# Performance work log

Hardware: AMD Instinct MI355X
Metric: run time of the kernel (lower is better)

The kernel has to match this reference:

```python
import jax, jax.numpy as jnp
import numpy as np

BATCH, N_AGENTS, OBS_DIM, ACTOR_DIM, N_ACTIONS = 8192, 64, 128, 64, 32


def setup_inputs() -> dict:
    key = jax.random.key(0)
    ks = jax.random.split(key, 14)
    s = 0.05
    inp = {
        "O": jax.random.normal(ks[0], (BATCH, N_AGENTS, OBS_DIM), dtype=jnp.float32),
        "W_enc": jax.random.normal(ks[1], (OBS_DIM, ACTOR_DIM), dtype=jnp.float32) * s,
        "b_enc": jax.random.normal(ks[2], (ACTOR_DIM,), dtype=jnp.float32) * s,
        "W1": jax.random.normal(ks[3], (2 * ACTOR_DIM, ACTOR_DIM), dtype=jnp.float32) * s,
        "b1": jax.random.normal(ks[4], (ACTOR_DIM,), dtype=jnp.float32) * s,
        "W2": jax.random.normal(ks[5], (2 * ACTOR_DIM, ACTOR_DIM), dtype=jnp.float32) * s,
        "b2": jax.random.normal(ks[6], (ACTOR_DIM,), dtype=jnp.float32) * s,
        "W3": jax.random.normal(ks[7], (2 * ACTOR_DIM, ACTOR_DIM), dtype=jnp.float32) * s,
        "b3": jax.random.normal(ks[8], (ACTOR_DIM,), dtype=jnp.float32) * s,
        "W4": jax.random.normal(ks[9], (2 * ACTOR_DIM, ACTOR_DIM), dtype=jnp.float32) * s,
        "b4": jax.random.normal(ks[10], (ACTOR_DIM,), dtype=jnp.float32) * s,
        "W_dec": jax.random.normal(ks[11], (N_AGENTS * ACTOR_DIM, N_ACTIONS), dtype=jnp.float32) * s,
        "b_dec": jax.random.normal(ks[12], (N_ACTIONS,), dtype=jnp.float32) * s,
    }
    return inp


def _comm_layer(H, W, b, n_agents):
    # get_commvar: masked mean over other agents, but divided by n_agents
    # (the zeroed self term is included in the mean denominator) ->
    # C_i = (sum_j H_j - H_i) / n_agents, exactly equal to the original math.
    C = (jnp.sum(H, axis=1, keepdims=True) - H) / n_agents  # [B, A, D]
    Hcat = jnp.concatenate([H, C], axis=-1)                 # [B, A, 2D]
    return Hcat @ W + b                                     # no activation (faithful)


def reference(O, W_enc, b_enc, W1, b1, W2, b2, W3, b3, W4, b4, W_dec, b_dec):
    B, A, _ = O.shape
    H = jax.nn.sigmoid(O @ W_enc + b_enc)  # [B, A, D]
    H = _comm_layer(H, W1, b1, A)
    H = _comm_layer(H, W2, b2, A)
    H = _comm_layer(H, W3, b3, A)
    H = _comm_layer(H, W4, b4, A)
    Hf = H.reshape(B, -1)                  # [B, A*D]
    return Hf @ W_dec + b_dec              # [B, n_actions]
```

## Files before the change

kernel.cpp:

```cpp
#include <hip/hip_runtime.h>
#include <hip/hip_bf16.h>
#include <stdint.h>


#define BATCHN 8192

typedef __attribute__((ext_vector_type(8))) short short8;
typedef __attribute__((ext_vector_type(4))) float floatx4;

__device__ __forceinline__ unsigned short f2b(float f) {
    union { float f; uint32_t u; } v; v.f = f;
    uint32_t r = v.u + 0x7FFFu + ((v.u >> 16) & 1u);
    return (unsigned short)(r >> 16);
}

__device__ __forceinline__ uint32_t pk2(float x, float y) {
    float2 t; t.x = x; t.y = y;
    __hip_bfloat162 h = __float22bfloat162_rn(t);
    union { __hip_bfloat162 h; uint32_t u; } c; c.h = h;
    return c.u;
}

#define U16_WENC 0
#define U16_WCAT 8192
#define U16_WSUM 40960
#define U16_WDEC 57344
#define U16_H4   188416

__global__ __launch_bounds__(256) void prep_kernel(
    const float* __restrict__ Wenc,
    const float* __restrict__ W1, const float* __restrict__ W2,
    const float* __restrict__ W3, const float* __restrict__ W4,
    const float* __restrict__ Wdec,
    unsigned short* __restrict__ ws)
{
    int tid = blockIdx.x * 256 + threadIdx.x;
    const float* WL[4] = {W1, W2, W3, W4};
    if (tid < 8192) {
        int n = tid >> 7, k = tid & 127;
        ws[U16_WENC + n*128 + k] = f2b(Wenc[k*64 + n]);
    } else if (tid < 40960) {
        int e = tid - 8192;
        int l = e >> 13, r = e & 8191;
        int n = r >> 7, k = r & 127;
        const float* W = WL[l];
        float v = W[k*64 + n];
        if (k < 64) v -= W[(k+64)*64 + n] * (1.0f/64.0f);
        ws[U16_WCAT + l*8192 + n*128 + k] = f2b(v);
    } else if (tid < 57344) {
        int e = tid - 40960;
        int l = e >> 12, r = e & 4095;
        int f = r >> 6, k = r & 63;
        const float* W = WL[l];
        float v = W[k*64 + f] + W[(k+64)*64 + f] * (63.0f/64.0f);
        ws[U16_WSUM + l*4096 + f*64 + k] = f2b(v);
    } else {
        int e = tid - 57344;
        int n = e >> 12, k = e & 4095;
        ws[U16_WDEC + n*4096 + k] = f2b(Wdec[k*32 + n]);
    }
}

__global__ __launch_bounds__(256, 3) void fused3_kernel(
    const float* __restrict__ O,
    const unsigned short* __restrict__ WencT,
    const unsigned short* __restrict__ WcatT,
    const unsigned short* __restrict__ WsumT,
    const float* __restrict__ b_enc,
    const float* __restrict__ b1, const float* __restrict__ b2,
    const float* __restrict__ b3, const float* __restrict__ b4,
    unsigned short* __restrict__ H4out)
{
    __shared__ unsigned short sG[4][64*72];
    __shared__ unsigned short sS[4][64];

    const int t = threadIdx.x, lane = t & 63, w = t >> 6;
    const int m = lane & 15, q = lane >> 4;
    const int b = blockIdx.x * 4 + w;
    unsigned short* myG = sG[w];
    unsigned short* myS = sS[w];

    floatx4 acc[4][4];
    floatx4 bb[4];

    #pragma unroll
    for (int ft = 0; ft < 4; ft++) {
        float4 bv = *(const float4*)(b_enc + ft*16 + q*4);
        bb[ft] = (floatx4){bv.x, bv.y, bv.z, bv.w};
    }
    #pragma unroll
    for (int ft = 0; ft < 4; ft++)
        #pragma unroll
        for (int at = 0; at < 4; at++)
            acc[ft][at] = bb[ft];

    const float* Ob = O + (size_t)b * 8192;
    #pragma unroll
    for (int s = 0; s < 4; s++) {
        short8 Wf[4], Bf[4];
        #pragma unroll
        for (int ft = 0; ft < 4; ft++)
            Wf[ft] = *(const short8*)(WencT + (ft*16+m)*128 + s*32 + q*8);
        #pragma unroll
        for (int at = 0; at < 4; at++) {
            const float* pr = Ob + (at*16+m)*128 + s*32 + q*8;
            float4 f0 = *(const float4*)pr;
            float4 f1 = *(const float4*)(pr + 4);
            uint32_t* pa = (uint32_t*)&Bf[at];
            pa[0] = pk2(f0.x, f0.y); pa[1] = pk2(f0.z, f0.w);
            pa[2] = pk2(f1.x, f1.y); pa[3] = pk2(f1.z, f1.w);
        }
        #pragma unroll
        for (int ft = 0; ft < 4; ft++)
            #pragma unroll
            for (int at = 0; at < 4; at++)
                acc[ft][at] = __builtin_amdgcn_mfma_f32_16x16x32_bf16(Wf[ft], Bf[at], acc[ft][at], 0, 0, 0);
    }
    #pragma unroll
    for (int ft = 0; ft < 4; ft++)
        #pragma unroll
        for (int at = 0; at < 4; at++)
            #pragma unroll
            for (int r = 0; r < 4; r++)
                acc[ft][at][r] = 1.0f / (1.0f + __expf(-acc[ft][at][r]));

    #pragma unroll
    for (int ft = 0; ft < 4; ft++) {
        float tr[4];
        #pragma unroll
        for (int r = 0; r < 4; r++)
            tr[r] = acc[ft][0][r] + acc[ft][1][r] + acc[ft][2][r] + acc[ft][3][r];
        #pragma unroll
        for (int msk = 1; msk <= 8; msk <<= 1)
            #pragma unroll
            for (int r = 0; r < 4; r++)
                tr[r] += __shfl_xor(tr[r], msk, 64);
        uint2 d;
        d.x = pk2(tr[0] * (1.0f/64.0f), tr[1] * (1.0f/64.0f));
        d.y = pk2(tr[2] * (1.0f/64.0f), tr[3] * (1.0f/64.0f));
        if (m == 0) *(uint2*)&myS[ft*16 + q*4] = d;
    }
    #pragma unroll
    for (int ft = 0; ft < 4; ft++)
        #pragma unroll
        for (int at = 0; at < 4; at++) {
            uint2 d;
            d.x = pk2(acc[ft][at][0], acc[ft][at][1]);
            d.y = pk2(acc[ft][at][2], acc[ft][at][3]);
            *(uint2*)&myG[(at*16+m)*72 + ft*16 + q*4] = d;
        }

    const float* bs_[4] = {b1, b2, b3, b4};
    #pragma unroll
    for (int l = 0; l < 4; l++) {
        const unsigned short* Wl  = WcatT + l*8192;
        const unsigned short* Wsl = WsumT + l*4096;
        const float* bp = bs_[l];
        #pragma unroll
        for (int ft = 0; ft < 4; ft++) {
            float4 bv = *(const float4*)(bp + ft*16 + q*4);
            bb[ft] = (floatx4){bv.x, bv.y, bv.z, bv.w};
        }
        short8 Sf[2];
        #pragma unroll
        for (int s2 = 0; s2 < 2; s2++)
            Sf[s2] = *(const short8*)&myS[s2*32 + q*8];

        #pragma unroll
        for (int ft = 0; ft < 4; ft++)
            #pragma unroll
            for (int at = 0; at < 4; at++)
                acc[ft][at] = bb[ft];

        #pragma unroll
        for (int s2 = 0; s2 < 2; s2++) {
            short8 Wf[4], Gf[4];
            #pragma unroll
            for (int ft = 0; ft < 4; ft++)
                Wf[ft] = *(const short8*)(Wl + (ft*16+m)*128 + s2*32 + q*8);
            #pragma unroll
            for (int at = 0; at < 4; at++)
                Gf[at] = *(const short8*)&myG[(at*16+m)*72 + s2*32 + q*8];
            #pragma unroll
            for (int ft = 0; ft < 4; ft++)
                #pragma unroll
                for (int at = 0; at < 4; at++)
                    acc[ft][at] = __builtin_amdgcn_mfma_f32_16x16x32_bf16(Wf[ft], Gf[at], acc[ft][at], 0, 0, 0);
        }
        #pragma unroll
        for (int s2 = 0; s2 < 2; s2++) {
            short8 Wf[4];
            #pragma unroll
            for (int ft = 0; ft < 4; ft++)
                Wf[ft] = *(const short8*)(Wl + (ft*16+m)*128 + (2+s2)*32 + q*8);
            #pragma unroll
            for (int ft = 0; ft < 4; ft++)
                #pragma unroll
                for (int at = 0; at < 4; at++)
                    acc[ft][at] = __builtin_amdgcn_mfma_f32_16x16x32_bf16(Wf[ft], Sf[s2], acc[ft][at], 0, 0, 0);
        }

        if (l < 3) {
            floatx4 sacc[4];
            #pragma unroll
            for (int ft = 0; ft < 4; ft++) sacc[ft] = (floatx4){0.f, 0.f, 0.f, 0.f};
            #pragma unroll
            for (int s2 = 0; s2 < 2; s2++) {
                #pragma unroll
                for (int ft = 0; ft < 4; ft++) {
                    short8 Wsf = *(const short8*)(Wsl + (ft*16+m)*64 + s2*32 + q*8);
                    sacc[ft] = __builtin_amdgcn_mfma_f32_16x16x32_bf16(Wsf, Sf[s2], sacc[ft], 0, 0, 0);
                }
            }
            #pragma unroll
            for (int ft = 0; ft < 4; ft++) {
                uint2 d;
                d.x = pk2(sacc[ft][0] + bb[ft][0], sacc[ft][1] + bb[ft][1]);
                d.y = pk2(sacc[ft][2] + bb[ft][2], sacc[ft][3] + bb[ft][3]);
                if (m == 0) *(uint2*)&myS[ft*16 + q*4] = d;
            }
            #pragma unroll
            for (int ft = 0; ft < 4; ft++)
                #pragma unroll
                for (int at = 0; at < 4; at++) {
                    uint2 d;
                    d.x = pk2(acc[ft][at][0], acc[ft][at][1]);
                    d.y = pk2(acc[ft][at][2], acc[ft][at][3]);
                    *(uint2*)&myG[(at*16+m)*72 + ft*16 + q*4] = d;
                }
        } else {
            unsigned short* Hb = H4out + (size_t)b * 4096;
            #pragma unroll
            for (int ft = 0; ft < 4; ft++)
                #pragma unroll
                for (int at = 0; at < 4; at++) {
                    uint2 d;
                    d.x = pk2(acc[ft][at][0], acc[ft][at][1]);
                    d.y = pk2(acc[ft][at][2], acc[ft][at][3]);
                    *(uint2*)(Hb + (at*16+m)*64 + ft*16 + q*4) = d;
                }
        }
    }
}

__global__ __launch_bounds__(256) void dec_kernel(
    const unsigned short* __restrict__ Hf,
    const unsigned short* __restrict__ WdecT,
    const float* __restrict__ b_dec,
    float* __restrict__ out)
{
    int gt = blockIdx.x * 256 + threadIdx.x;
    int wave = gt >> 6;
    int lane = gt & 63;
    int rb = wave >> 3;
    int kc = wave & 7;
    int m = lane & 15, q = lane >> 4;

    const unsigned short* aP  = Hf    + (size_t)(rb*16 + m)*4096 + kc*512 + q*8;
    const unsigned short* bP0 = WdecT + (size_t)m*4096        + kc*512 + q*8;
    const unsigned short* bP1 = WdecT + (size_t)(16 + m)*4096 + kc*512 + q*8;

    floatx4 a0 = {0.f, 0.f, 0.f, 0.f}, a1 = {0.f, 0.f, 0.f, 0.f};
    #pragma unroll 4
    for (int s = 0; s < 16; s++) {
        short8 av  = *(const short8*)(aP  + s*32);
        short8 b0v = *(const short8*)(bP0 + s*32);
        short8 b1v = *(const short8*)(bP1 + s*32);
        a0 = __builtin_amdgcn_mfma_f32_16x16x32_bf16(av, b0v, a0, 0, 0, 0);
        a1 = __builtin_amdgcn_mfma_f32_16x16x32_bf16(av, b1v, a1, 0, 0, 0);
    }
    float bias0 = (kc == 0) ? b_dec[m]      : 0.0f;
    float bias1 = (kc == 0) ? b_dec[16 + m] : 0.0f;
    #pragma unroll
    for (int r = 0; r < 4; r++) {
        int row = rb*16 + q*4 + r;
        atomicAdd(&out[row*32 + m],      a0[r] + bias0);
        atomicAdd(&out[row*32 + 16 + m], a1[r] + bias1);
    }
}

extern "C" void kernel_launch(void* const* d_in, const int* in_sizes, int n_in,
                              void* d_out, int out_size, void* d_ws, size_t ws_size,
                              hipStream_t stream)
{
    const float* O    = (const float*)d_in[0];
    const float* Wenc = (const float*)d_in[1];
    const float* benc = (const float*)d_in[2];
    const float* W1   = (const float*)d_in[3];
    const float* b1   = (const float*)d_in[4];
    const float* W2   = (const float*)d_in[5];
    const float* b2   = (const float*)d_in[6];
    const float* W3   = (const float*)d_in[7];
    const float* b3   = (const float*)d_in[8];
    const float* W4   = (const float*)d_in[9];
    const float* b4   = (const float*)d_in[10];
    const float* Wdec = (const float*)d_in[11];
    const float* bdec = (const float*)d_in[12];
    float* out = (float*)d_out;
    unsigned short* ws = (unsigned short*)d_ws;

    hipMemsetAsync(d_out, 0, (size_t)out_size * sizeof(float), stream);
    prep_kernel<<<736, 256, 0, stream>>>(Wenc, W1, W2, W3, W4, Wdec, ws);
    fused3_kernel<<<2048, 256, 0, stream>>>(O, ws + U16_WENC, ws + U16_WCAT,
                                            ws + U16_WSUM,
                                            benc, b1, b2, b3, b4, ws + U16_H4);
    dec_kernel<<<1024, 256, 0, stream>>>(ws + U16_H4, ws + U16_WDEC, bdec, out);
}
```

Before: 502.0 us.

## Prefetch encoder inputs, reorder comm-layer loads, replace decoder atomics with partial-sum reduction

The encoder loop now double-buffers the fp32 observation loads, fetching the next K-slice while the current one is converted and multiplied. Each comm layer loads all G fragments and weights up front and computes the summary vector before the main MFMA block. The decoder splits K into 16 chunks that write partial sums to workspace instead of using atomics, and a new reduction kernel adds the bias and sums the partials. This removes the memset and the atomic contention, at the cost of an extra launch, 16 MB of partial traffic and higher register pressure.

New measurement: 499.9 us. Within noise of the previous version (-0.4%).

```diff
diff --git a/kernel.cpp b/kernel.cpp
--- a/kernel.cpp
+++ b/kernel.cpp
@@ -26,6 +26,7 @@
 #define U16_WSUM 40960
 #define U16_WDEC 57344
 #define U16_H4   188416
+#define F32_PART 16871424
 
 __global__ __launch_bounds__(256) void prep_kernel(
     const float* __restrict__ Wenc,
@@ -61,7 +62,7 @@
     }
 }
 
-__global__ __launch_bounds__(256, 3) void fused3_kernel(
+__global__ __launch_bounds__(256, 3) void fused4_kernel(
     const float* __restrict__ O,
     const unsigned short* __restrict__ WencT,
     const unsigned short* __restrict__ WcatT,
@@ -95,17 +96,30 @@
             acc[ft][at] = bb[ft];
 
     const float* Ob = O + (size_t)b * 8192;
+    float4 stg[2][4][2];
+    #pragma unroll
+    for (int at = 0; at < 4; at++) {
+        const float* pr = Ob + (at*16+m)*128 + q*8;
+        stg[0][at][0] = *(const float4*)pr;
+        stg[0][at][1] = *(const float4*)(pr + 4);
+    }
     #pragma unroll
     for (int s = 0; s < 4; s++) {
+        if (s < 3) {
+            #pragma unroll
+            for (int at = 0; at < 4; at++) {
+                const float* pr = Ob + (at*16+m)*128 + (s+1)*32 + q*8;
+                stg[(s+1)&1][at][0] = *(const float4*)pr;
+                stg[(s+1)&1][at][1] = *(const float4*)(pr + 4);
+            }
+        }
         short8 Wf[4], Bf[4];
         #pragma unroll
         for (int ft = 0; ft < 4; ft++)
             Wf[ft] = *(const short8*)(WencT + (ft*16+m)*128 + s*32 + q*8);
         #pragma unroll
         for (int at = 0; at < 4; at++) {
-            const float* pr = Ob + (at*16+m)*128 + s*32 + q*8;
-            float4 f0 = *(const float4*)pr;
-            float4 f1 = *(const float4*)(pr + 4);
+            float4 f0 = stg[s&1][at][0], f1 = stg[s&1][at][1];
             uint32_t* pa = (uint32_t*)&Bf[at];
             pa[0] = pk2(f0.x, f0.y); pa[1] = pk2(f0.z, f0.w);
             pa[2] = pk2(f1.x, f1.y); pa[3] = pk2(f1.z, f1.w);
@@ -165,60 +179,61 @@
         #pragma unroll
         for (int s2 = 0; s2 < 2; s2++)
             Sf[s2] = *(const short8*)&myS[s2*32 + q*8];
-
-        #pragma unroll
-        for (int ft = 0; ft < 4; ft++)
+        short8 Gf[2][4];
+        #pragma unroll
+        for (int s2 = 0; s2 < 2; s2++)
             #pragma unroll
             for (int at = 0; at < 4; at++)
-                acc[ft][at] = bb[ft];
-
-        #pragma unroll
-        for (int s2 = 0; s2 < 2; s2++) {
-            short8 Wf[4], Gf[4];
-            #pragma unroll
-            for (int ft = 0; ft < 4; ft++)
-                Wf[ft] = *(const short8*)(Wl + (ft*16+m)*128 + s2*32 + q*8);
-            #pragma unroll
-            for (int at = 0; at < 4; at++)
-                Gf[at] = *(const short8*)&myG[(at*16+m)*72 + s2*32 + q*8];
-            #pragma unroll
-            for (int ft = 0; ft < 4; ft++)
-                #pragma unroll
-                for (int at = 0; at < 4; at++)
-                    acc[ft][at] = __builtin_amdgcn_mfma_f32_16x16x32_bf16(Wf[ft], Gf[at], acc[ft][at], 0, 0, 0);
-        }
-        #pragma unroll
-        for (int s2 = 0; s2 < 2; s2++) {
-            short8 Wf[4];
-            #pragma unroll
-            for (int ft = 0; ft < 4; ft++)
-                Wf[ft] = *(const short8*)(Wl + (ft*16+m)*128 + (2+s2)*32 + q*8);
-            #pragma unroll
-            for (int ft = 0; ft < 4; ft++)
-                #pragma unroll
-                for (int at = 0; at < 4; at++)
-                    acc[ft][at] = __builtin_amdgcn_mfma_f32_16x16x32_bf16(Wf[ft], Sf[s2], acc[ft][at], 0, 0, 0);
-        }
+                Gf[s2][at] = *(const short8*)&myG[(at*16+m)*72 + s2*32 + q*8];
+
+        short8 Wk[4][4];
+        #pragma unroll
+        for (int s = 0; s < 4; s++)
+            #pragma unroll
+            for (int ft = 0; ft < 4; ft++)
+                Wk[s][ft] = *(const short8*)(Wl + (ft*16+m)*128 + s*32 + q*8);
 
         if (l < 3) {
             floatx4 sacc[4];
             #pragma unroll
-            for (int ft = 0; ft < 4; ft++) sacc[ft] = (floatx4){0.f, 0.f, 0.f, 0.f};
-            #pragma unroll
-            for (int s2 = 0; s2 < 2; s2++) {
+            for (int ft = 0; ft < 4; ft++) sacc[ft] = bb[ft];
+            #pragma unroll
+            for (int s2 = 0; s2 < 2; s2++)
                 #pragma unroll
                 for (int ft = 0; ft < 4; ft++) {
                     short8 Wsf = *(const short8*)(Wsl + (ft*16+m)*64 + s2*32 + q*8);
                     sacc[ft] = __builtin_amdgcn_mfma_f32_16x16x32_bf16(Wsf, Sf[s2], sacc[ft], 0, 0, 0);
                 }
-            }
             #pragma unroll
             for (int ft = 0; ft < 4; ft++) {
                 uint2 d;
-                d.x = pk2(sacc[ft][0] + bb[ft][0], sacc[ft][1] + bb[ft][1]);
-                d.y = pk2(sacc[ft][2] + bb[ft][2], sacc[ft][3] + bb[ft][3]);
+                d.x = pk2(sacc[ft][0], sacc[ft][1]);
+                d.y = pk2(sacc[ft][2], sacc[ft][3]);
                 if (m == 0) *(uint2*)&myS[ft*16 + q*4] = d;
             }
+        }
+
+        #pragma unroll
+        for (int ft = 0; ft < 4; ft++)
+            #pragma unroll
+            for (int at = 0; at < 4; at++)
+                acc[ft][at] = bb[ft];
+        #pragma unroll
+        for (int s2 = 0; s2 < 2; s2++)
+            #pragma unroll
+            for (int ft = 0; ft < 4; ft++)
+                #pragma unroll
+                for (int at = 0; at < 4; at++)
+                    acc[ft][at] = __builtin_amdgcn_mfma_f32_16x16x32_bf16(Wk[s2][ft], Gf[s2][at], acc[ft][at], 0, 0, 0);
+        #pragma unroll
+        for (int s2 = 0; s2 < 2; s2++)
+            #pragma unroll
+            for (int ft = 0; ft < 4; ft++)
+                #pragma unroll
+                for (int at = 0; at < 4; at++)
+                    acc[ft][at] = __builtin_amdgcn_mfma_f32_16x16x32_bf16(Wk[2+s2][ft], Sf[s2], acc[ft][at], 0, 0, 0);
+
+        if (l < 3) {
             #pragma unroll
             for (int ft = 0; ft < 4; ft++)
                 #pragma unroll
@@ -243,40 +258,53 @@
     }
 }
 
-__global__ __launch_bounds__(256) void dec_kernel(
+__global__ __launch_bounds__(256, 4) void dec_kernel(
     const unsigned short* __restrict__ Hf,
     const unsigned short* __restrict__ WdecT,
-    const float* __restrict__ b_dec,
-    float* __restrict__ out)
+    float* __restrict__ P)
 {
     int gt = blockIdx.x * 256 + threadIdx.x;
     int wave = gt >> 6;
     int lane = gt & 63;
-    int rb = wave >> 3;
-    int kc = wave & 7;
+    int rb = wave >> 4;
+    int kc = wave & 15;
     int m = lane & 15, q = lane >> 4;
 
-    const unsigned short* aP  = Hf    + (size_t)(rb*16 + m)*4096 + kc*512 + q*8;
-    const unsigned short* bP0 = WdecT + (size_t)m*4096        + kc*512 + q*8;
-    const unsigned short* bP1 = WdecT + (size_t)(16 + m)*4096 + kc*512 + q*8;
+    const unsigned short* aP  = Hf    + (size_t)(rb*16 + m)*4096 + kc*256 + q*8;
+    const unsigned short* bP0 = WdecT + (size_t)m*4096        + kc*256 + q*8;
+    const unsigned short* bP1 = WdecT + (size_t)(16 + m)*4096 + kc*256 + q*8;
 
     floatx4 a0 = {0.f, 0.f, 0.f, 0.f}, a1 = {0.f, 0.f, 0.f, 0.f};
-    #pragma unroll 4
-    for (int s = 0; s < 16; s++) {
+    #pragma unroll
+    for (int s = 0; s < 8; s++) {
         short8 av  = *(const short8*)(aP  + s*32);
         short8 b0v = *(const short8*)(bP0 + s*32);
         short8 b1v = *(const short8*)(bP1 + s*32);
         a0 = __builtin_amdgcn_mfma_f32_16x16x32_bf16(av, b0v, a0, 0, 0, 0);
         a1 = __builtin_amdgcn_mfma_f32_16x16x32_bf16(av, b1v, a1, 0, 0, 0);
     }
-    float bias0 = (kc == 0) ? b_dec[m]      : 0.0f;
-    float bias1 = (kc == 0) ? b_dec[16 + m] : 0.0f;
+    float* Pk = P + (size_t)kc * (8192*32);
     #pragma unroll
     for (int r = 0; r < 4; r++) {
         int row = rb*16 + q*4 + r;
-        atomicAdd(&out[row*32 + m],      a0[r] + bias0);
-        atomicAdd(&out[row*32 + 16 + m], a1[r] + bias1);
-    }
+        Pk[row*32 + m]      = a0[r];
+        Pk[row*32 + 16 + m] = a1[r];
+    }
+}
+
+__global__ __launch_bounds__(256) void red_kernel(
+    const float* __restrict__ P, const float* __restrict__ b_dec,
+    float* __restrict__ out)
+{
+    int tid = blockIdx.x * 256 + threadIdx.x;
+    float4 bv = *(const float4*)(b_dec + (tid & 7) * 4);
+    float4 s = bv;
+    #pragma unroll
+    for (int kc = 0; kc < 16; kc++) {
+        float4 v = *(const float4*)(P + (size_t)kc * (8192*32) + tid*4);
+        s.x += v.x; s.y += v.y; s.z += v.z; s.w += v.w;
+    }
+    *(float4*)(out + tid*4) = s;
 }
 
 extern "C" void kernel_launch(void* const* d_in, const int* in_sizes, int n_in,
@@ -298,11 +326,12 @@
     const float* bdec = (const float*)d_in[12];
     float* out = (float*)d_out;
     unsigned short* ws = (unsigned short*)d_ws;
-
-    hipMemsetAsync(d_out, 0, (size_t)out_size * sizeof(float), stream);
+    float* wsf = (float*)d_ws;
+
     prep_kernel<<<736, 256, 0, stream>>>(Wenc, W1, W2, W3, W4, Wdec, ws);
-    fused3_kernel<<<2048, 256, 0, stream>>>(O, ws + U16_WENC, ws + U16_WCAT,
+    fused4_kernel<<<2048, 256, 0, stream>>>(O, ws + U16_WENC, ws + U16_WCAT,
                                             ws + U16_WSUM,
                                             benc, b1, b2, b3, b4, ws + U16_H4);
-    dec_kernel<<<1024, 256, 0, stream>>>(ws + U16_H4, ws + U16_WDEC, bdec, out);
-}
+    dec_kernel<<<2048, 256, 0, stream>>>(ws + U16_H4, ws + U16_WDEC, wsf + F32_PART);
+    red_kernel<<<256, 256, 0, stream>>>(wsf + F32_PART, bdec, out);
+}
```
